# Kernel optimization log

Hardware: AMD Instinct MI355X
Metric: run time of the kernel (lower is better)

The kernel has to match this reference:

```python
import jax, jax.numpy as jnp
import numpy as np

D_MODEL = 512; NHEAD = 8; HEAD = D_MODEL // NHEAD
DFF = 2048; K = 31; T = 512; B = 16
EPS = float(np.exp(0.25))  # BasicNorm eps stored in log space, init 0.25


def setup_inputs():
    key = jax.random.key(0)
    ks = jax.random.split(key, 24)
    def rn(k, shape, scale):
        return jax.random.normal(k, shape, jnp.float32) * scale
    si = 1.0 / np.sqrt(D_MODEL); sf = 1.0 / np.sqrt(DFF); sk = 1.0 / np.sqrt(K)
    return {
        "src": jax.random.normal(ks[0], (T, B, D_MODEL), jnp.float32),
        "pos_emb": jax.random.normal(ks[1], (1, 2 * T - 1, D_MODEL), jnp.float32),
        "ffm_w1": rn(ks[2], (DFF, D_MODEL), si), "ffm_b1": jnp.zeros((DFF,), jnp.float32),
        "ffm_w2": rn(ks[3], (D_MODEL, DFF), 0.25 * sf), "ffm_b2": jnp.zeros((D_MODEL,), jnp.float32),
        "ff_w1": rn(ks[4], (DFF, D_MODEL), si), "ff_b1": jnp.zeros((DFF,), jnp.float32),
        "ff_w2": rn(ks[5], (D_MODEL, DFF), 0.25 * sf), "ff_b2": jnp.zeros((D_MODEL,), jnp.float32),
        "in_proj_w": rn(ks[6], (3 * D_MODEL, D_MODEL), si), "in_proj_b": jnp.zeros((3 * D_MODEL,), jnp.float32),
        "out_proj_w": rn(ks[7], (D_MODEL, D_MODEL), 0.25 * si), "out_proj_b": jnp.zeros((D_MODEL,), jnp.float32),
        "linear_pos_w": rn(ks[8], (D_MODEL, D_MODEL), si),
        "pos_bias_u": rn(ks[9], (NHEAD, HEAD), 0.01),
        "pos_bias_v": rn(ks[10], (NHEAD, HEAD), 0.01),
        "conv_pw1_w": rn(ks[11], (2 * D_MODEL, D_MODEL), si), "conv_pw1_b": jnp.zeros((2 * D_MODEL,), jnp.float32),
        "conv_dw_w": rn(ks[12], (D_MODEL, K), sk), "conv_dw_b": jnp.zeros((D_MODEL,), jnp.float32),
        "conv_pw2_w": rn(ks[13], (D_MODEL, D_MODEL), 0.25 * si), "conv_pw2_b": jnp.zeros((D_MODEL,), jnp.float32),
    }


def _double_swish(x):
    return x * jax.nn.sigmoid(x - 1.0)


def _rel_shift(x):
    # x: (B, H, T, 2T-1) -> (B, H, T, T); out[..., i, j] = x[..., i, T-1-i+j]
    t = x.shape[2]
    idx = (t - 1) - jnp.arange(t)[:, None] + jnp.arange(t)[None, :]
    return jnp.take_along_axis(x, idx[None, None], axis=-1)


def reference(src, pos_emb, ffm_w1, ffm_b1, ffm_w2, ffm_b2, ff_w1, ff_b1, ff_w2, ff_b2,
              in_proj_w, in_proj_b, out_proj_w, out_proj_b, linear_pos_w, pos_bias_u, pos_bias_v,
              conv_pw1_w, conv_pw1_b, conv_dw_w, conv_dw_b, conv_pw2_w, conv_pw2_b):
    t, b, c = src.shape
    h, d = pos_bias_u.shape

    def ffw(x, w1, b1, w2, b2):  # ScaledLinear -> DoubleSwish -> ScaledLinear
        return _double_swish(x @ w1.T + b1) @ w2.T + b2

    # macaron feed-forward (ActivationBalancer/Dropout are identity in fwd/eval)
    x = src + ffw(src, ffm_w1, ffm_b1, ffm_w2, ffm_b2)

    # rel-pos self-attention
    qkv = x @ in_proj_w.T + in_proj_b  # (T,B,3C)
    q, k, v = jnp.split(qkv, 3, axis=-1)
    q = (q * (d ** -0.5)).reshape(t, b, h, d).transpose(1, 2, 0, 3)  # (B,H,T,d)
    k = k.reshape(t, b, h, d).transpose(1, 2, 0, 3)
    v = v.reshape(t, b, h, d).transpose(1, 2, 0, 3)
    p = (pos_emb @ linear_pos_w.T).reshape(-1, 2 * t - 1, h, d)[0].transpose(1, 0, 2)  # (H,2T-1,d)
    ac = jnp.einsum('bhtd,bhsd->bhts', q + pos_bias_u[None, :, None, :], k)
    bd = _rel_shift(jnp.einsum('bhtd,hpd->bhtp', q + pos_bias_v[None, :, None, :], p))
    attn = jax.nn.softmax(ac + bd, axis=-1)
    ao = jnp.einsum('bhts,bhsd->bhtd', attn, v).transpose(2, 0, 1, 3).reshape(t, b, c)
    x = x + (ao @ out_proj_w.T + out_proj_b)

    # causal convolution module
    xc = x.transpose(1, 2, 0)  # (B,C,T)
    xc = jnp.einsum('oc,bct->bot', conv_pw1_w, xc) + conv_pw1_b[None, :, None]  # (B,2C,T)
    a, g = jnp.split(xc, 2, axis=1)
    xc = a * jax.nn.sigmoid(g)  # GLU over channel dim
    xc = jnp.pad(xc, ((0, 0), (0, 0), (K - 1, 0)))  # zero cache = causal left pad
    xc = jax.lax.conv_general_dilated(xc, conv_dw_w[:, None, :], (1,), 'VALID',
                                      dimension_numbers=('NCH', 'OIH', 'NCH'),
                                      feature_group_count=c) + conv_dw_b[None, :, None]
    xc = _double_swish(xc)
    xc = jnp.einsum('oc,bct->bot', conv_pw2_w, xc) + conv_pw2_b[None, :, None]
    x = x + xc.transpose(2, 0, 1)

    # second feed-forward
    x = x + ffw(x, ff_w1, ff_b1, ff_w2, ff_b2)

    # BasicNorm over channel dim (balancer is identity in forward)
    x = x * jax.lax.rsqrt(jnp.mean(x * x, axis=-1, keepdims=True) + EPS)
    return x
```

## Files before the change

### kernel.cpp

```cpp
#include <hip/hip_runtime.h>
#include <math.h>

#define T_SEQ 512
#define B_SZ  16
#define C_DIM 512
#define NH    8
#define HD    64
#define DFF_  2048
#define NROWS (T_SEQ * B_SZ)
#define EPS_BN 1.2840254166877414f

typedef unsigned short u16;
typedef __attribute__((ext_vector_type(8))) short bf16x8;
typedef __attribute__((ext_vector_type(4))) float f32x4;

__device__ __forceinline__ float sigmoidf_(float x) { return 1.f / (1.f + __expf(-x)); }
__device__ __forceinline__ float dswishf_(float x)  { return x * sigmoidf_(x - 1.f); }
__device__ __forceinline__ float clampd_(float x)   { return fminf(fmaxf(x, -1e4f), 1e4f); }
__device__ __forceinline__ u16 f2bf_(float x) {
    unsigned u = __float_as_uint(x);
    return (u16)((u + 0x7fffu + ((u >> 16) & 1u)) >> 16);
}
__device__ __forceinline__ float bf2f_(u16 u) {
    return __uint_as_float(((unsigned)u) << 16);
}

template <int ACT, bool HAS_RES, bool O32, bool O16>
__global__ __launch_bounds__(512) void gemm_mfma(
    const u16* __restrict__ A, const u16* __restrict__ W,
    const float* __restrict__ bias, const float* __restrict__ res,
    float* __restrict__ out32, u16* __restrict__ out16, int N, int K, int M)
{
    __shared__ __align__(16) u16 As[2][128 * 32];
    __shared__ __align__(16) u16 Bs[2][128 * 32];
    const int tid  = threadIdx.x;
    const int wv   = tid >> 6;
    const int lane = tid & 63;
    const int wm   = wv >> 2, wn = wv & 3;
    const int m0 = blockIdx.x * 128;
    const int n0 = blockIdx.y * 128;

    const int sc_ = tid & 3;
    const int sr_ = tid >> 2;
    const u16* gA = A + (size_t)(n0 + sr_) * K + sc_ * 8;
    const u16* gB = W + (size_t)(m0 + sr_) * K + sc_ * 8;
    const int ls = sr_ * 32 + sc_ * 8;

    f32x4 acc[4][2];
#pragma unroll
    for (int i = 0; i < 4; ++i)
#pragma unroll
        for (int j = 0; j < 2; ++j) acc[i][j] = (f32x4)0.f;

    const int frow = (lane & 15);
    const int fk   = (lane >> 4) * 8;

    uint4 ra = *(const uint4*)(gA);
    uint4 rb = *(const uint4*)(gB);
    *(uint4*)&As[0][ls] = ra;
    *(uint4*)&Bs[0][ls] = rb;
    __syncthreads();

    int buf = 0;
    for (int k0 = 0; k0 < K; k0 += 32) {
        const bool last = (k0 + 32 >= K);
        if (!last) {
            ra = *(const uint4*)(gA + k0 + 32);
            rb = *(const uint4*)(gB + k0 + 32);
        }
        bf16x8 af[4], bf[2];
#pragma unroll
        for (int i = 0; i < 4; ++i)
            af[i] = *(const bf16x8*)&As[buf][(wm * 64 + i * 16 + frow) * 32 + fk];
#pragma unroll
        for (int j = 0; j < 2; ++j)
            bf[j] = *(const bf16x8*)&Bs[buf][(wn * 32 + j * 16 + frow) * 32 + fk];
#pragma unroll
        for (int i = 0; i < 4; ++i)
#pragma unroll
            for (int j = 0; j < 2; ++j)
                acc[i][j] = __builtin_amdgcn_mfma_f32_16x16x32_bf16(af[i], bf[j], acc[i][j], 0, 0, 0);
        if (!last) {
            const int nb = buf ^ 1;
            *(uint4*)&As[nb][ls] = ra;
            *(uint4*)&Bs[nb][ls] = rb;
            __syncthreads();
            buf = nb;
        }
    }

    const int quad = lane >> 4;
#pragma unroll
    for (int i = 0; i < 4; ++i) {
        const int row = n0 + wm * 64 + i * 16 + quad * 4;
#pragma unroll
        for (int j = 0; j < 2; ++j) {
            const int col = m0 + wn * 32 + j * 16 + (lane & 15);
            const float bv = bias ? bias[col] : 0.f;
#pragma unroll
            for (int r = 0; r < 4; ++r) {
                float v = acc[i][j][r] + bv;
                if (ACT == 1) v = dswishf_(v);
                if (HAS_RES) v += res[(size_t)(row + r) * M + col];
                v = clampd_(v);
                if (O32) out32[(size_t)(row + r) * M + col] = v;
                if (O16) out16[(size_t)(row + r) * M + col] = f2bf_(v);
            }
        }
    }
}

template <int EPI>
__global__ __launch_bounds__(512) void gemm_fused(
    const u16* __restrict__ A, const u16* __restrict__ W,
    const float* __restrict__ bias, const float* __restrict__ ub, const float* __restrict__ vb,
    u16* __restrict__ o_qu, u16* __restrict__ o_qv, u16* __restrict__ o_k,
    u16* __restrict__ o_v, u16* __restrict__ o_p, int N, int K, int M)
{
    __shared__ __align__(16) u16 As[2][128 * 32];
    __shared__ __align__(16) u16 Bs[2][128 * 32];
    const int tid  = threadIdx.x;
    const int wv   = tid >> 6;
    const int lane = tid & 63;
    const int wm   = wv >> 2, wn = wv & 3;
    const int m0 = blockIdx.x * 128;
    const int n0 = blockIdx.y * 128;

    const int sc_ = tid & 3;
    const int sr_ = tid >> 2;
    const u16* gA = A + (size_t)(n0 + sr_) * K + sc_ * 8;
    const u16* gB = W + (size_t)(m0 + sr_) * K + sc_ * 8;
    const int ls = sr_ * 32 + sc_ * 8;

    f32x4 acc[4][2];
#pragma unroll
    for (int i = 0; i < 4; ++i)
#pragma unroll
        for (int j = 0; j < 2; ++j) acc[i][j] = (f32x4)0.f;

    const int frow = (lane & 15);
    const int fk   = (lane >> 4) * 8;

    uint4 ra = *(const uint4*)(gA);
    uint4 rb = *(const uint4*)(gB);
    *(uint4*)&As[0][ls] = ra;
    *(uint4*)&Bs[0][ls] = rb;
    __syncthreads();

    int buf = 0;
    for (int k0 = 0; k0 < K; k0 += 32) {
        const bool last = (k0 + 32 >= K);
        if (!last) {
            ra = *(const uint4*)(gA + k0 + 32);
            rb = *(const uint4*)(gB + k0 + 32);
        }
        bf16x8 af[4], bf[2];
#pragma unroll
        for (int i = 0; i < 4; ++i)
            af[i] = *(const bf16x8*)&As[buf][(wm * 64 + i * 16 + frow) * 32 + fk];
#pragma unroll
        for (int j = 0; j < 2; ++j)
            bf[j] = *(const bf16x8*)&Bs[buf][(wn * 32 + j * 16 + frow) * 32 + fk];
#pragma unroll
        for (int i = 0; i < 4; ++i)
#pragma unroll
            for (int j = 0; j < 2; ++j)
                acc[i][j] = __builtin_amdgcn_mfma_f32_16x16x32_bf16(af[i], bf[j], acc[i][j], 0, 0, 0);
        if (!last) {
            const int nb = buf ^ 1;
            *(uint4*)&As[nb][ls] = ra;
            *(uint4*)&Bs[nb][ls] = rb;
            __syncthreads();
            buf = nb;
        }
    }

    const int quad = lane >> 4;
#pragma unroll
    for (int i = 0; i < 4; ++i) {
        const int rowb = n0 + wm * 64 + i * 16 + quad * 4;
#pragma unroll
        for (int j = 0; j < 2; ++j) {
            const int col = m0 + wn * 32 + j * 16 + (lane & 15);
            if (EPI == 0) {
                const float bv = bias[col];
                const int c = col & 511, h = c >> 6, d = c & 63;
#pragma unroll
                for (int r = 0; r < 4; ++r) {
                    const int row = rowb + r;
                    const float v = clampd_(acc[i][j][r] + bv);
                    const int t = row >> 4, b = row & 15;
                    const size_t dst = ((size_t)(b * 8 + h) * 512 + t) * 64 + d;
                    if (col < 512) {
                        o_qu[dst] = f2bf_(v * 0.125f + ub[c]);
                        o_qv[dst] = f2bf_(v * 0.125f + vb[c]);
                    } else if (col < 1024) {
                        o_k[dst] = f2bf_(v);
                    } else {
                        o_v[dst] = f2bf_(v);
                    }
                }
            } else {
                const int h = col >> 6, d = col & 63;
#pragma unroll
                for (int r = 0; r < 4; ++r)
                    o_p[(size_t)h * 65536 + (size_t)(rowb + r) * 64 + d] = f2bf_(acc[i][j][r]);
            }
        }
    }
}

__device__ __forceinline__ void store_bf4_(u16* out, float4 v) {
    const unsigned lo = (unsigned)f2bf_(v.x) | ((unsigned)f2bf_(v.y) << 16);
    const unsigned hi = (unsigned)f2bf_(v.z) | ((unsigned)f2bf_(v.w) << 16);
    *(uint2*)out = make_uint2(lo, hi);
}

__global__ __launch_bounds__(256) void cvt_k(const float* __restrict__ in, u16* __restrict__ out)
{
    const int i4 = (blockIdx.x * 256 + threadIdx.x) * 4;
    store_bf4_(out + i4, *(const float4*)(in + i4));
}

struct WPtrs { const float* p[9]; };
__global__ __launch_bounds__(256) void cvt_w_k(WPtrs wp, u16* __restrict__ out)
{
    static const int off[10] = {0, 1048576, 2097152, 3145728, 4194304,
                                4980736, 5242880, 5505024, 6029312, 6291456};
    const int e = (blockIdx.x * 256 + threadIdx.x) * 4;
    int r = 0;
#pragma unroll
    for (int k = 1; k < 9; ++k) r += (e >= off[k]);
    store_bf4_(out + e, *(const float4*)(wp.p[r] + (e - off[r])));
}

__global__ __launch_bounds__(256) void cvt_pos_k(const float* __restrict__ in, u16* __restrict__ out)
{
    const int e = (blockIdx.x * 256 + threadIdx.x) * 4;
    float4 v = make_float4(0.f, 0.f, 0.f, 0.f);
    if (e < 1023 * 512) v = *(const float4*)(in + e);
    store_bf4_(out + e, v);
}

__global__ __launch_bounds__(256) void vt_k(const u16* __restrict__ in, u16* __restrict__ out)
{
    __shared__ u16 tile[64][65];
    const int s0 = blockIdx.x * 64;
    const int gbh = blockIdx.y;
    const u16* src = in + (size_t)gbh * 512 * 64;
    u16* dst = out + (size_t)gbh * 64 * 512;
    const int tid = threadIdx.x;
#pragma unroll
    for (int q = 0; q < 2; ++q) {
        const int lin = tid * 2 + q;
        const int srow = lin >> 3, c8 = (lin & 7) * 8;
        const uint4 v = *(const uint4*)(src + (size_t)(s0 + srow) * 64 + c8);
        const u16* vu = (const u16*)&v;
#pragma unroll
        for (int e = 0; e < 8; ++e) tile[srow][c8 + e] = vu[e];
    }
    __syncthreads();
#pragma unroll
    for (int q = 0; q < 2; ++q) {
        const int lin = tid * 2 + q;
        const int d = lin >> 3, sc8 = (lin & 7) * 8;
        u16 o[8];
#pragma unroll
        for (int e = 0; e < 8; ++e) o[e] = tile[sc8 + e][d];
        *(uint4*)(dst + (size_t)d * 512 + s0 + sc8) = *(uint4*)o;
    }
}

#define C2S 88
#define PS  72
__global__ __launch_bounds__(256, 4) void flash_attn(
    const u16* __restrict__ qu_b, const u16* __restrict__ qv_b,
    const u16* __restrict__ k_b, const u16* __restrict__ vt_b,
    const u16* __restrict__ p_b, u16* __restrict__ aob)
{
    __shared__ __align__(16) u16 C2ld[4][16 * C2S];
    __shared__ __align__(16) u16 Pld[4][16 * PS];
    const int tid = threadIdx.x;
    const int wv = tid >> 6;
    const int lane = tid & 63;
    const int quad = lane >> 4, ln = lane & 15;
    const int gbh = blockIdx.y;
    const int b = gbh >> 3, h = gbh & 7;
    const int t0 = blockIdx.x * 64 + wv * 16;

    const u16* qu = qu_b + (size_t)gbh * 512 * 64;
    const u16* qv = qv_b + (size_t)gbh * 512 * 64;
    const u16* kb = k_b + (size_t)gbh * 512 * 64;
    const u16* vt = vt_b + (size_t)gbh * 64 * 512;
    const u16* pp = p_b + (size_t)h * 1024 * 64;

    bf16x8 aqu[2], aqv[2];
#pragma unroll
    for (int ks = 0; ks < 2; ++ks) {
        aqu[ks] = *(const bf16x8*)(qu + (size_t)(t0 + ln) * 64 + ks * 32 + quad * 8);
        aqv[ks] = *(const bf16x8*)(qv + (size_t)(t0 + ln) * 64 + ks * 32 + quad * 8);
    }

    const short ob = (short)0x3F80;
    const bf16x8 vone = {ob, ob, ob, ob, ob, ob, ob, ob};

    f32x4 O[4];
#pragma unroll
    for (int nb = 0; nb < 4; ++nb) O[nb] = (f32x4)0.f;
    f32x4 Lacc = (f32x4)0.f;
    float m[4];
#pragma unroll
    for (int r = 0; r < 4; ++r) m[r] = -1e30f;

    u16* c2w = &C2ld[wv][0];
    u16* pw  = &Pld[wv][0];

    for (int s0 = 0; s0 < 512; s0 += 64) {
        f32x4 S[4];
#pragma unroll
        for (int nb = 0; nb < 4; ++nb) S[nb] = (f32x4)0.f;
        __builtin_amdgcn_s_setprio(1);
#pragma unroll
        for (int ks = 0; ks < 2; ++ks)
#pragma unroll
            for (int nb = 0; nb < 4; ++nb) {
                const bf16x8 bk = *(const bf16x8*)(kb + (size_t)(s0 + nb * 16 + ln) * 64 + ks * 32 + quad * 8);
                S[nb] = __builtin_amdgcn_mfma_f32_16x16x32_bf16(aqu[ks], bk, S[nb], 0, 0, 0);
            }
        __builtin_amdgcn_s_setprio(0);
        const int jlo = 496 - t0 + s0;
        f32x4 C2[5];
#pragma unroll
        for (int nb = 0; nb < 5; ++nb) C2[nb] = (f32x4)0.f;
        __builtin_amdgcn_s_setprio(1);
#pragma unroll
        for (int ks = 0; ks < 2; ++ks)
#pragma unroll
            for (int nb = 0; nb < 5; ++nb) {
                const bf16x8 bp = *(const bf16x8*)(pp + (size_t)(jlo + nb * 16 + ln) * 64 + ks * 32 + quad * 8);
                C2[nb] = __builtin_amdgcn_mfma_f32_16x16x32_bf16(aqv[ks], bp, C2[nb], 0, 0, 0);
            }
        __builtin_amdgcn_s_setprio(0);
#pragma unroll
        for (int nb = 0; nb < 5; ++nb)
#pragma unroll
            for (int r = 0; r < 4; ++r)
                c2w[(quad * 4 + r) * C2S + nb * 16 + ln] = f2bf_(C2[nb][r]);

        float sv[4][4];
        float rmax[4] = {-1e30f, -1e30f, -1e30f, -1e30f};
#pragma unroll
        for (int nb = 0; nb < 4; ++nb)
#pragma unroll
            for (int r = 0; r < 4; ++r) {
                const int tloc = quad * 4 + r;
                const int col = nb * 16 + ln + 15 - tloc;
                const float bd = bf2f_(c2w[tloc * C2S + col]);
                const float s = clampd_(S[nb][r] + bd);
                sv[nb][r] = s;
                rmax[r] = fmaxf(rmax[r], s);
            }
#pragma unroll
        for (int off = 1; off < 16; off <<= 1)
#pragma unroll
            for (int r = 0; r < 4; ++r)
                rmax[r] = fmaxf(rmax[r], __shfl_xor(rmax[r], off, 64));

        float alpha[4];
#pragma unroll
        for (int r = 0; r < 4; ++r) {
            const float mn = fmaxf(m[r], rmax[r]);
            alpha[r] = __expf(m[r] - mn);
            m[r] = mn;
        }
#pragma unroll
        for (int nb = 0; nb < 4; ++nb)
#pragma unroll
            for (int r = 0; r < 4; ++r) {
                const float p = __expf(sv[nb][r] - m[r]);
                pw[(quad * 4 + r) * PS + nb * 16 + ln] = f2bf_(p);
            }
#pragma unroll
        for (int nb = 0; nb < 4; ++nb)
#pragma unroll
            for (int r = 0; r < 4; ++r) O[nb][r] *= alpha[r];
#pragma unroll
        for (int r = 0; r < 4; ++r) Lacc[r] *= alpha[r];

        __builtin_amdgcn_s_setprio(1);
#pragma unroll
        for (int ks = 0; ks < 2; ++ks) {
            const bf16x8 ap = *(const bf16x8*)&pw[ln * PS + ks * 32 + quad * 8];
#pragma unroll
            for (int nb = 0; nb < 4; ++nb) {
                const bf16x8 bv = *(const bf16x8*)(vt + (size_t)(nb * 16 + ln) * 512 + s0 + ks * 32 + quad * 8);
                O[nb] = __builtin_amdgcn_mfma_f32_16x16x32_bf16(ap, bv, O[nb], 0, 0, 0);
            }
            Lacc = __builtin_amdgcn_mfma_f32_16x16x32_bf16(ap, vone, Lacc, 0, 0, 0);
        }
        __builtin_amdgcn_s_setprio(0);
    }

    float inv[4];
#pragma unroll
    for (int r = 0; r < 4; ++r) inv[r] = 1.f / Lacc[r];
#pragma unroll
    for (int nb = 0; nb < 4; ++nb)
#pragma unroll
        for (int r = 0; r < 4; ++r) {
            const int t = t0 + quad * 4 + r;
            const int d = nb * 16 + ln;
            aob[((size_t)t * B_SZ + b) * 512 + h * 64 + d] = f2bf_(O[nb][r] * inv[r]);
        }
}

__global__ __launch_bounds__(256) void glu_k(const u16* __restrict__ in, u16* __restrict__ out)
{
    const int i4 = (blockIdx.x * 256 + threadIdx.x) * 4;
    const int n = i4 >> 9, c = i4 & 511;
    const uint2 av = *(const uint2*)(in + (size_t)n * 1024 + c);
    const uint2 gv = *(const uint2*)(in + (size_t)n * 1024 + 512 + c);
    const u16* au = (const u16*)&av;
    const u16* gu = (const u16*)&gv;
    u16 o[4];
#pragma unroll
    for (int q = 0; q < 4; ++q) {
        const float a = bf2f_(au[q]), g = bf2f_(gu[q]);
        o[q] = f2bf_(a * sigmoidf_(g));
    }
    *(uint2*)(out + i4) = *(uint2*)o;
}

__global__ __launch_bounds__(256) void dwt_k(const float* __restrict__ w, float* __restrict__ wT)
{
    const int idx = blockIdx.x * 256 + threadIdx.x;
    if (idx >= 31 * 512) return;
    const int j = idx >> 9, c = idx & 511;
    wT[idx] = w[c * 31 + j];
}

__global__ __launch_bounds__(256) void dwconv_k(
    const u16* __restrict__ g, const float* __restrict__ wT,
    const float* __restrict__ bb, u16* __restrict__ out)
{
    const int idx = blockIdx.x * 256 + threadIdx.x;
    const int c = idx & 511;
    const int b = (idx >> 9) & 15;
    const int t0 = (idx >> 13) * 8;
    float wr[31];
#pragma unroll
    for (int j = 0; j < 31; ++j) wr[j] = wT[j * 512 + c];
    float win[38];
#pragma unroll
    for (int jj = 0; jj < 38; ++jj) {
        const int tt = t0 - 30 + jj;
        win[jj] = (tt >= 0) ? bf2f_(g[((size_t)tt * B_SZ + b) * 512 + c]) : 0.f;
    }
    const float bias = bb[c];
#pragma unroll
    for (int o = 0; o < 8; ++o) {
        float acc = bias;
#pragma unroll
        for (int j = 0; j < 31; ++j) acc += win[o + j] * wr[j];
        out[((size_t)(t0 + o) * B_SZ + b) * 512 + c] = f2bf_(dswishf_(acc));
    }
}

__global__ __launch_bounds__(256) void norm_k(float* __restrict__ x)
{
    const int row = blockIdx.x * 4 + (threadIdx.x >> 6);
    const int lane = threadIdx.x & 63;
    float* r = x + (size_t)row * 512;
    float v[8];
    float ss = 0.f;
#pragma unroll
    for (int j = 0; j < 8; ++j) { v[j] = r[lane + (j << 6)]; ss += v[j] * v[j]; }
#pragma unroll
    for (int o = 32; o > 0; o >>= 1) ss += __shfl_xor(ss, o, 64);
    const float scale = rsqrtf(ss * (1.f / 512.f) + EPS_BN);
#pragma unroll
    for (int j = 0; j < 8; ++j) r[lane + (j << 6)] = v[j] * scale;
}

extern "C" void kernel_launch(void* const* d_in, const int* in_sizes, int n_in,
                              void* d_out, int out_size, void* d_ws, size_t ws_size,
                              hipStream_t stream)
{
    const float* src   = (const float*)d_in[0];
    const float* pos   = (const float*)d_in[1];
    const float* fm_w1 = (const float*)d_in[2];
    const float* fm_b1 = (const float*)d_in[3];
    const float* fm_w2 = (const float*)d_in[4];
    const float* fm_b2 = (const float*)d_in[5];
    const float* f_w1  = (const float*)d_in[6];
    const float* f_b1  = (const float*)d_in[7];
    const float* f_w2  = (const float*)d_in[8];
    const float* f_b2  = (const float*)d_in[9];
    const float* ipw   = (const float*)d_in[10];
    const float* ipb   = (const float*)d_in[11];
    const float* opw   = (const float*)d_in[12];
    const float* opb   = (const float*)d_in[13];
    const float* lpw   = (const float*)d_in[14];
    const float* pbu   = (const float*)d_in[15];
    const float* pbv   = (const float*)d_in[16];
    const float* cpw1  = (const float*)d_in[17];
    const float* cpb1  = (const float*)d_in[18];
    const float* cdw   = (const float*)d_in[19];
    const float* cdb   = (const float*)d_in[20];
    const float* cpw2  = (const float*)d_in[21];
    const float* cpb2  = (const float*)d_in[22];

    float* x = (float*)d_out;

    char* base = (char*)d_ws;
    u16*   wb    = (u16*)base;   base += 6291456ull * 2;
    u16*   src_b = (u16*)base;   base += 4194304ull * 2;
    u16*   pos_b = (u16*)base;   base += 524288ull * 2;
    u16*   xb    = (u16*)base;   base += 4194304ull * 2;
    u16*   hb    = (u16*)base;   base += 16777216ull * 2;
    u16*   aob   = (u16*)base;   base += 4194304ull * 2;
    u16*   qu_b  = (u16*)base;   base += 4194304ull * 2;
    u16*   qv_b  = (u16*)base;   base += 4194304ull * 2;
    u16*   k_b   = (u16*)base;   base += 4194304ull * 2;
    u16*   v_b   = (u16*)base;   base += 4194304ull * 2;
    u16*   vt_b  = (u16*)base;   base += 4194304ull * 2;
    u16*   p_b   = (u16*)base;   base += 524288ull * 2;
    float* wTd   = (float*)base; base += 15872ull * 4;
    u16*   pw1_o = (u16*)base;   base += 8388608ull * 2;
    u16*   glu_o = (u16*)base;   base += 4194304ull * 2;

    u16* fm_w1b = wb;
    u16* fm_w2b = wb + 1048576;
    u16* f_w1b  = wb + 2097152;
    u16* f_w2b  = wb + 3145728;
    u16* ipwb   = wb + 4194304;
    u16* opwb   = wb + 4980736;
    u16* lpwb   = wb + 5242880;
    u16* cpw1b  = wb + 5505024;
    u16* cpw2b  = wb + 6029312;

    const dim3 blk(256);
    const dim3 blkg(512);

    WPtrs wp = {{fm_w1, fm_w2, f_w1, f_w2, ipw, opw, lpw, cpw1, cpw2}};
    cvt_w_k<<<dim3(6291456 / 1024), blk, 0, stream>>>(wp, wb);
    cvt_k<<<dim3(4194304 / 1024), blk, 0, stream>>>(src, src_b);
    cvt_pos_k<<<dim3(524288 / 1024), blk, 0, stream>>>(pos, pos_b);
    dwt_k<<<dim3(62), blk, 0, stream>>>(cdw, wTd);

    gemm_mfma<1, false, false, true><<<dim3(16, 64), blkg, 0, stream>>>(
        src_b, fm_w1b, fm_b1, nullptr, nullptr, hb, NROWS, 512, DFF_);
    gemm_mfma<0, true, true, true><<<dim3(4, 64), blkg, 0, stream>>>(
        hb, fm_w2b, fm_b2, src, x, xb, NROWS, DFF_, 512);

    gemm_fused<0><<<dim3(12, 64), blkg, 0, stream>>>(
        xb, ipwb, ipb, pbu, pbv, qu_b, qv_b, k_b, v_b, nullptr, NROWS, 512, 1536);
    gemm_fused<1><<<dim3(4, 8), blkg, 0, stream>>>(
        pos_b, lpwb, nullptr, nullptr, nullptr,
        nullptr, nullptr, nullptr, nullptr, p_b, 1024, 512, 512);
    vt_k<<<dim3(8, 128), blk, 0, stream>>>(v_b, vt_b);

    flash_attn<<<dim3(8, 128), blk, 0, stream>>>(qu_b, qv_b, k_b, vt_b, p_b, aob);

    gemm_mfma<0, true, true, true><<<dim3(4, 64), blkg, 0, stream>>>(
        aob, opwb, opb, x, x, xb, NROWS, 512, 512);

    gemm_mfma<0, false, false, true><<<dim3(8, 64), blkg, 0, stream>>>(
        xb, cpw1b, cpb1, nullptr, nullptr, pw1_o, NROWS, 512, 1024);
    glu_k<<<dim3(NROWS * 512 / 1024), blk, 0, stream>>>(pw1_o, glu_o);
    dwconv_k<<<dim3(2048), blk, 0, stream>>>(glu_o, wTd, cdb, hb);
    gemm_mfma<0, true, true, true><<<dim3(4, 64), blkg, 0, stream>>>(
        hb, cpw2b, cpb2, x, x, xb, NROWS, 512, 512);

    gemm_mfma<1, false, false, true><<<dim3(16, 64), blkg, 0, stream>>>(
        xb, f_w1b, f_b1, nullptr, nullptr, hb, NROWS, 512, DFF_);
    gemm_mfma<0, true, true, false><<<dim3(4, 64), blkg, 0, stream>>>(
        hb, f_w2b, f_b2, x, x, nullptr, NROWS, DFF_, 512);

    norm_k<<<dim3(NROWS / 4), blk, 0, stream>>>(x);
}
```

Before: 494.5 us.

## Split attention key range across two blocks and merge partials in combine kernel

The flash attention kernel gets a z grid dimension that splits the 512 keys into two halves. Each half writes unnormalized fp32 outputs plus its running max and sum into scratch buffers that reuse existing allocations, and a new combine kernel merges them with the log-sum-exp rescaling. The aim is to double the number of blocks (1024 to 2048) and raise the occupancy hint to 8 waves per SIMD, so the GPU is better filled. In exchange it adds fp32 partial-result traffic, an extra kernel launch, and tighter register limits.

```diff
diff --git a/kernel.cpp b/kernel.cpp
--- a/kernel.cpp
+++ b/kernel.cpp
@@ -273,10 +273,10 @@
 
 #define C2S 88
 #define PS  72
-__global__ __launch_bounds__(256, 4) void flash_attn(
+__global__ __launch_bounds__(256, 8) void flash_attn(
     const u16* __restrict__ qu_b, const u16* __restrict__ qv_b,
     const u16* __restrict__ k_b, const u16* __restrict__ vt_b,
-    const u16* __restrict__ p_b, u16* __restrict__ aob)
+    const u16* __restrict__ p_b, float* __restrict__ po, float* __restrict__ pml)
 {
     __shared__ __align__(16) u16 C2ld[4][16 * C2S];
     __shared__ __align__(16) u16 Pld[4][16 * PS];
@@ -285,7 +285,8 @@
     const int lane = tid & 63;
     const int quad = lane >> 4, ln = lane & 15;
     const int gbh = blockIdx.y;
-    const int b = gbh >> 3, h = gbh & 7;
+    const int h = gbh & 7;
+    const int shalf = blockIdx.z;
     const int t0 = blockIdx.x * 64 + wv * 16;
 
     const u16* qu = qu_b + (size_t)gbh * 512 * 64;
@@ -315,7 +316,8 @@
     u16* c2w = &C2ld[wv][0];
     u16* pw  = &Pld[wv][0];
 
-    for (int s0 = 0; s0 < 512; s0 += 64) {
+    const int sbase = shalf << 8;
+    for (int s0 = sbase; s0 < sbase + 256; s0 += 64) {
         f32x4 S[4];
 #pragma unroll
         for (int nb = 0; nb < 4; ++nb) S[nb] = (f32x4)0.f;
@@ -401,17 +403,46 @@
         __builtin_amdgcn_s_setprio(0);
     }
 
-    float inv[4];
-#pragma unroll
-    for (int r = 0; r < 4; ++r) inv[r] = 1.f / Lacc[r];
+    float* po_w  = po  + ((size_t)(shalf * 128 + gbh) * 512) * 64;
+    float* pml_w = pml + ((size_t)(shalf * 128 + gbh) * 512) * 2;
 #pragma unroll
     for (int nb = 0; nb < 4; ++nb)
 #pragma unroll
         for (int r = 0; r < 4; ++r) {
             const int t = t0 + quad * 4 + r;
-            const int d = nb * 16 + ln;
-            aob[((size_t)t * B_SZ + b) * 512 + h * 64 + d] = f2bf_(O[nb][r] * inv[r]);
-        }
+            po_w[(size_t)t * 64 + nb * 16 + ln] = O[nb][r];
+        }
+    if (ln == 0) {
+#pragma unroll
+        for (int r = 0; r < 4; ++r) {
+            const int t = t0 + quad * 4 + r;
+            pml_w[t * 2]     = m[r];
+            pml_w[t * 2 + 1] = Lacc[r];
+        }
+    }
+}
+
+__global__ __launch_bounds__(256) void fa_combine_k(
+    const float* __restrict__ po, const float* __restrict__ pml, u16* __restrict__ aob)
+{
+    const int idx = blockIdx.x * 256 + threadIdx.x;
+    const int row = idx >> 4;
+    const int d4  = (idx & 15) * 4;
+    const float4 o0 = *(const float4*)(po + (size_t)row * 64 + d4);
+    const float4 o1 = *(const float4*)(po + (size_t)(row + 65536) * 64 + d4);
+    const float m0 = pml[(size_t)row * 2],           L0 = pml[(size_t)row * 2 + 1];
+    const float m1 = pml[(size_t)(row + 65536) * 2], L1 = pml[(size_t)(row + 65536) * 2 + 1];
+    const float mn = fmaxf(m0, m1);
+    const float a0 = __expf(m0 - mn), a1 = __expf(m1 - mn);
+    const float inv = 1.f / (L0 * a0 + L1 * a1);
+    float4 o;
+    o.x = (o0.x * a0 + o1.x * a1) * inv;
+    o.y = (o0.y * a0 + o1.y * a1) * inv;
+    o.z = (o0.z * a0 + o1.z * a1) * inv;
+    o.w = (o0.w * a0 + o1.w * a1) * inv;
+    const int gbh = row >> 9, t = row & 511;
+    const int b = gbh >> 3, h = gbh & 7;
+    store_bf4_(aob + ((size_t)t * B_SZ + b) * 512 + h * 64 + d4, o);
 }
 
 __global__ __launch_bounds__(256) void glu_k(const u16* __restrict__ in, u16* __restrict__ out)
@@ -539,6 +570,9 @@
     u16* cpw1b  = wb + 5505024;
     u16* cpw2b  = wb + 6029312;
 
+    float* po  = (float*)hb;
+    float* pml = (float*)pw1_o;
+
     const dim3 blk(256);
     const dim3 blkg(512);
 
@@ -560,7 +594,8 @@
         nullptr, nullptr, nullptr, nullptr, p_b, 1024, 512, 512);
     vt_k<<<dim3(8, 128), blk, 0, stream>>>(v_b, vt_b);
 
-    flash_attn<<<dim3(8, 128), blk, 0, stream>>>(qu_b, qv_b, k_b, vt_b, p_b, aob);
+    flash_attn<<<dim3(8, 128, 2), blk, 0, stream>>>(qu_b, qv_b, k_b, vt_b, p_b, po, pml);
+    fa_combine_k<<<dim3(4096), blk, 0, stream>>>(po, pml, aob);
 
     gemm_mfma<0, true, true, true><<<dim3(4, 64), blkg, 0, stream>>>(
         aob, opwb, opb, x, x, xb, NROWS, 512, 512);
```

After: 582.9 us. 17.9% more time.
